# Kernel tuning notes

Measured on AMD Instinct MI355X. Metric: run time of the kernel, lower is better.

Reference implementation:

```python
import jax, jax.numpy as jnp
import numpy as np

IN_FEATURES = 4096
OUT_FEATURES = 4096
BATCH, SEQ = 4, 2048

def setup_inputs() -> dict:
    key = jax.random.key(0)
    k1, k2, k3, k4, k5 = jax.random.split(key, 5)
    x = jax.random.normal(k1, (BATCH, SEQ, IN_FEATURES), dtype=jnp.float32)
    # int8 codes stored as int32 in [0, 255] (asymmetric uint8-style quantization)
    qweight = jax.random.randint(k2, (OUT_FEATURES, IN_FEATURES), 0, 255, dtype=jnp.int32)
    scales = jax.random.uniform(k3, (OUT_FEATURES,), dtype=jnp.float32) * 0.01 + 1e-3
    zero_points = jax.random.uniform(k4, (OUT_FEATURES,), dtype=jnp.float32) * 255.0
    bias = jax.random.normal(k5, (OUT_FEATURES,), dtype=jnp.float32)
    return {"x": x, "qweight": qweight, "scales": scales, "zero_points": zero_points, "bias": bias}

def reference(x, qweight, scales, zero_points, bias):
    # Per-output-channel dequantization: W[o, i] = (q[o, i] - zp[o]) * scale[o]
    w = (qweight.astype(jnp.float32) - zero_points[:, None]) * scales[:, None]  # [O, I]
    # y = x @ W.T + b, fused dequant + GEMM in the original ipex op
    y = jnp.einsum("bsi,oi->bso", x, w) + bias
    return y
```

## Files before the change

### kernel.cpp

```cpp
#include <hip/hip_runtime.h>
#include <hip/hip_bf16.h>

typedef __attribute__((ext_vector_type(4))) int i32x4;
typedef __attribute__((ext_vector_type(16))) int i32x16;

#define M_DIM 8192
#define N_DIM 4096
#define K_DIM 4096
#define BM 256
#define BN 256
#define BK 64
#define NT2 (K_DIM / BK)

static __device__ inline void gload_lds16(const void* g, void* l) {
  __builtin_amdgcn_global_load_lds(
      (const __attribute__((address_space(1))) unsigned int*)g,
      (__attribute__((address_space(3))) unsigned int*)l,
      16, 0, 0);
}

__global__ __launch_bounds__(256) void prep_x_i8(
    const float* __restrict__ x, char* __restrict__ xq,
    float* __restrict__ rx, float* __restrict__ sxf) {
  const int row = blockIdx.x;
  const int tid = threadIdx.x;
  const float4* xr = (const float4*)(x + (long)row * K_DIM);
  float4 v[4];
  float mx = 0.f;
#pragma unroll
  for (int i = 0; i < 4; ++i) {
    v[i] = xr[i * 256 + tid];
    mx = fmaxf(mx, fmaxf(fmaxf(fabsf(v[i].x), fabsf(v[i].y)),
                         fmaxf(fabsf(v[i].z), fabsf(v[i].w))));
  }
#pragma unroll
  for (int off = 32; off > 0; off >>= 1) mx = fmaxf(mx, __shfl_down(mx, off, 64));
  __shared__ float redm[4];
  __shared__ int reds[4];
  const int lane = tid & 63, w = tid >> 6;
  if (lane == 0) redm[w] = mx;
  __syncthreads();
  const float maxv = fmaxf(fmaxf(redm[0], redm[1]), fmaxf(redm[2], redm[3]));
  const float inv = maxv > 0.f ? 127.f / maxv : 0.f;
  int* xo = (int*)(xq + (long)row * K_DIM);
  int ssum = 0;
#pragma unroll
  for (int i = 0; i < 4; ++i) {
    const int q0 = __float2int_rn(v[i].x * inv);
    const int q1 = __float2int_rn(v[i].y * inv);
    const int q2 = __float2int_rn(v[i].z * inv);
    const int q3 = __float2int_rn(v[i].w * inv);
    ssum += q0 + q1 + q2 + q3;
    xo[i * 256 + tid] =
        (q0 & 255) | ((q1 & 255) << 8) | ((q2 & 255) << 16) | ((q3 & 255) << 24);
  }
#pragma unroll
  for (int off = 32; off > 0; off >>= 1) ssum += __shfl_down(ssum, off, 64);
  if (lane == 0) reds[w] = ssum;
  __syncthreads();
  if (tid == 0) {
    rx[row] = maxv * (1.f / 127.f);
    sxf[row] = (float)(reds[0] + reds[1] + reds[2] + reds[3]);
  }
}

__global__ __launch_bounds__(256) void prep_q_i8(
    const int* __restrict__ q, char* __restrict__ qb) {
  const long idx = (long)blockIdx.x * blockDim.x + threadIdx.x;
  const int4 v = ((const int4*)q)[idx];
  const int a = v.x - 128, b = v.y - 128, c = v.z - 128, d = v.w - 128;
  ((int*)qb)[idx] = (a & 255) | ((b & 255) << 8) | ((c & 255) << 16) | ((d & 255) << 24);
}

__global__ __launch_bounds__(512, 2) void wq_gemm_i8(
    const char* __restrict__ A,
    const char* __restrict__ B,
    const float* __restrict__ rx,
    const float* __restrict__ sxf,
    const float* __restrict__ scales,
    const float* __restrict__ zps,
    const float* __restrict__ bias,
    float* __restrict__ C) {
  __shared__ __align__(16) char lds[4 * 32768];

  const int tid = threadIdx.x;
  const int lane = tid & 63;
  const int wv = tid >> 6;
  const int wr = wv >> 2, wc = wv & 3;

  const int wg = blockIdx.x;
  const int lid = (wg & 7) * 64 + (wg >> 3);
  const int bx = lid & 15, by = lid >> 4;
  const int brow = by * BM;
  const int bcol = bx * BN;

  i32x16 acc[4][2] = {};

  const int srow = tid >> 2;
  const int schunk = ((tid & 3) ^ (srow & 3)) * 16;
  const int wub = (tid & ~63) * 16;
  const char* gAs = A + (long)(brow + srow) * K_DIM + schunk;
  const char* gBs = B + (long)(bcol + srow) * K_DIM + schunk;

#define STAGE_A(T)                                                        \
  do {                                                                    \
    char* d = lds + ((T) & 3) * 32768;                                    \
    gload_lds16(gAs + (long)(T) * 64, d + wub);                           \
    gload_lds16(gAs + 524288 + (long)(T) * 64, d + 8192 + wub);           \
  } while (0)
#define STAGE_B(T)                                                        \
  do {                                                                    \
    char* d = lds + ((T) & 3) * 32768 + 16384;                            \
    gload_lds16(gBs + (long)(T) * 64, d + wub);                           \
    gload_lds16(gBs + 524288 + (long)(T) * 64, d + 8192 + wub);           \
  } while (0)

  const int row5 = lane & 31;
  const int kg = lane >> 5;
  int aoff[2], boff[2];
#pragma unroll
  for (int ks = 0; ks < 2; ++ks) {
    const int ch = ((ks * 2 + kg) ^ (row5 & 3)) * 16;
    aoff[ks] = (wr * 128 + row5) * 64 + ch;
    boff[ks] = (wc * 64 + row5) * 64 + ch;
  }

#define RD_A(BB, FM, KS) (*(const i32x4*)(lds + (BB) + aoff[KS] + (FM) * 2048))
#define RD_B(BB, FN, KS) (*(const i32x4*)(lds + (BB) + 16384 + boff[KS] + (FN) * 2048))
#define MMA(FM, FN, AV, BV)                                                   \
  acc[FM][FN] = __builtin_amdgcn_mfma_i32_32x32x32_i8(AV, BV, acc[FM][FN], 0, 0, 0)

#define BAR() __builtin_amdgcn_s_barrier()
#define VMC(N)                                                                \
  do {                                                                        \
    asm volatile("s_waitcnt vmcnt(" #N ")");                                  \
    __builtin_amdgcn_sched_barrier(0);                                        \
  } while (0)

  STAGE_A(0); STAGE_B(0);
  STAGE_A(1); STAGE_B(1);
  VMC(4);
  BAR();

  i32x4 a00, a01, a10, a11, b00, b01, b10, b11;

  for (int t = 0; t < NT2 - 2; ++t) {
    const int bb = (t & 3) * 32768;
    a00 = RD_A(bb, 0, 0); a01 = RD_A(bb, 0, 1);
    a10 = RD_A(bb, 1, 0); a11 = RD_A(bb, 1, 1);
    b00 = RD_B(bb, 0, 0); b01 = RD_B(bb, 0, 1);
    b10 = RD_B(bb, 1, 0); b11 = RD_B(bb, 1, 1);
    STAGE_A(t + 2);
    BAR();
    __builtin_amdgcn_s_setprio(1);
    MMA(0, 0, a00, b00); MMA(0, 1, a00, b10);
    MMA(1, 0, a10, b00); MMA(1, 1, a10, b10);
    MMA(0, 0, a01, b01); MMA(0, 1, a01, b11);
    MMA(1, 0, a11, b01); MMA(1, 1, a11, b11);
    __builtin_amdgcn_s_setprio(0);
    BAR();
    a00 = RD_A(bb, 2, 0); a01 = RD_A(bb, 2, 1);
    a10 = RD_A(bb, 3, 0); a11 = RD_A(bb, 3, 1);
    STAGE_B(t + 2);
    BAR();
    __builtin_amdgcn_s_setprio(1);
    MMA(2, 0, a00, b00); MMA(2, 1, a00, b10);
    MMA(3, 0, a10, b00); MMA(3, 1, a10, b10);
    MMA(2, 0, a01, b01); MMA(2, 1, a01, b11);
    MMA(3, 0, a11, b01); MMA(3, 1, a11, b11);
    __builtin_amdgcn_s_setprio(0);
    VMC(4);
    BAR();
  }

#pragma unroll
  for (int tt = 0; tt < 2; ++tt) {
    const int t = NT2 - 2 + tt;
    const int bb = (t & 3) * 32768;
    a00 = RD_A(bb, 0, 0); a01 = RD_A(bb, 0, 1);
    a10 = RD_A(bb, 1, 0); a11 = RD_A(bb, 1, 1);
    b00 = RD_B(bb, 0, 0); b01 = RD_B(bb, 0, 1);
    b10 = RD_B(bb, 1, 0); b11 = RD_B(bb, 1, 1);
    MMA(0, 0, a00, b00); MMA(0, 1, a00, b10);
    MMA(1, 0, a10, b00); MMA(1, 1, a10, b10);
    MMA(0, 0, a01, b01); MMA(0, 1, a01, b11);
    MMA(1, 0, a11, b01); MMA(1, 1, a11, b11);
    a00 = RD_A(bb, 2, 0); a01 = RD_A(bb, 2, 1);
    a10 = RD_A(bb, 3, 0); a11 = RD_A(bb, 3, 1);
    MMA(2, 0, a00, b00); MMA(2, 1, a00, b10);
    MMA(3, 0, a10, b00); MMA(3, 1, a10, b10);
    MMA(2, 0, a01, b01); MMA(2, 1, a01, b11);
    MMA(3, 0, a11, b01); MMA(3, 1, a11, b11);
    if (tt == 0) { VMC(0); BAR(); }
  }

  float sc[2], zp[2], bs[2];
  int coln[2];
#pragma unroll
  for (int fn = 0; fn < 2; ++fn) {
    coln[fn] = bcol + wc * 64 + fn * 32 + row5;
    sc[fn] = scales[coln[fn]];
    zp[fn] = 128.f - zps[coln[fn]];
    bs[fn] = bias[coln[fn]];
  }
#pragma unroll
  for (int fm = 0; fm < 4; ++fm) {
#pragma unroll
    for (int r = 0; r < 16; ++r) {
      const int grow = brow + wr * 128 + fm * 32 + (r & 3) + 8 * (r >> 2) + 4 * kg;
      const float rxv = rx[grow];
      const float sxv = sxf[grow];
#pragma unroll
      for (int fn = 0; fn < 2; ++fn) {
        C[(long)grow * N_DIM + coln[fn]] =
            sc[fn] * rxv * ((float)acc[fm][fn][r] + zp[fn] * sxv) + bs[fn];
      }
    }
  }
}

extern "C" void kernel_launch(void* const* d_in, const int* in_sizes, int n_in,
                              void* d_out, int out_size, void* d_ws, size_t ws_size,
                              hipStream_t stream) {
  const float* x = (const float*)d_in[0];
  const int* qw = (const int*)d_in[1];
  const float* scales = (const float*)d_in[2];
  const float* zps = (const float*)d_in[3];
  const float* bias = (const float*)d_in[4];
  float* out = (float*)d_out;

  char* ws = (char*)d_ws;
  char* xq = ws;
  char* qb = ws + (size_t)32 * 1024 * 1024;
  float* rx = (float*)(ws + (size_t)48 * 1024 * 1024);
  float* sxf = (float*)(ws + (size_t)48 * 1024 * 1024 + 65536);

  hipLaunchKernelGGL(prep_x_i8, dim3(M_DIM), dim3(256), 0, stream, x, xq, rx, sxf);
  hipLaunchKernelGGL(prep_q_i8, dim3((N_DIM * K_DIM / 4) / 256), dim3(256), 0, stream,
                     qw, qb);
  hipLaunchKernelGGL(wq_gemm_i8, dim3((M_DIM / BM) * (N_DIM / BN)), dim3(512), 0,
                     stream, xq, qb, rx, sxf, scales, zps, bias, out);
}
```

Measured before the change: 215.6 us.

## Double K tile to 128 with two-stage LDS ring and finer-grained staging

Raises the GEMM K-tile from 64 to 128 and switches the LDS ring from four 32KB stages to two 64KB stages, with an 8-way XOR swizzle to match the wider rows. Each iteration now runs four MMA phases, and the global-to-LDS loads for the next tile are split into four quarter-stages placed between them. The aim is to halve the number of loop iterations and barriers per K element and to spread memory traffic more evenly across the compute. The cost is a shallower prefetch distance (one tile ahead instead of two), more live B registers, and subtler vmcnt and barrier ordering that could stall or race.

```diff
diff --git a/kernel.cpp b/kernel.cpp
--- a/kernel.cpp
+++ b/kernel.cpp
@@ -9,7 +9,7 @@
 #define K_DIM 4096
 #define BM 256
 #define BN 256
-#define BK 64
+#define BK 128
 #define NT2 (K_DIM / BK)
 
 static __device__ inline void gload_lds16(const void* g, void* l) {
@@ -81,7 +81,7 @@
     const float* __restrict__ zps,
     const float* __restrict__ bias,
     float* __restrict__ C) {
-  __shared__ __align__(16) char lds[4 * 32768];
+  __shared__ __align__(16) char lds[2 * 65536];
 
   const int tid = threadIdx.x;
   const int lane = tid & 63;
@@ -96,37 +96,41 @@
 
   i32x16 acc[4][2] = {};
 
-  const int srow = tid >> 2;
-  const int schunk = ((tid & 3) ^ (srow & 3)) * 16;
+  const int srow = tid >> 3;
+  const int schunk = ((tid & 7) ^ (srow & 7)) * 16;
   const int wub = (tid & ~63) * 16;
   const char* gAs = A + (long)(brow + srow) * K_DIM + schunk;
   const char* gBs = B + (long)(bcol + srow) * K_DIM + schunk;
 
-#define STAGE_A(T)                                                        \
-  do {                                                                    \
-    char* d = lds + ((T) & 3) * 32768;                                    \
-    gload_lds16(gAs + (long)(T) * 64, d + wub);                           \
-    gload_lds16(gAs + 524288 + (long)(T) * 64, d + 8192 + wub);           \
+#define STAGE_A2(T, J0, J1)                                                   \
+  do {                                                                        \
+    char* d = lds + ((T) & 1) * 65536;                                        \
+    gload_lds16(gAs + (long)(J0) * 262144 + (long)(T) * 128,                  \
+                d + (J0) * 8192 + wub);                                       \
+    gload_lds16(gAs + (long)(J1) * 262144 + (long)(T) * 128,                  \
+                d + (J1) * 8192 + wub);                                       \
   } while (0)
-#define STAGE_B(T)                                                        \
-  do {                                                                    \
-    char* d = lds + ((T) & 3) * 32768 + 16384;                            \
-    gload_lds16(gBs + (long)(T) * 64, d + wub);                           \
-    gload_lds16(gBs + 524288 + (long)(T) * 64, d + 8192 + wub);           \
+#define STAGE_B2(T, J0, J1)                                                   \
+  do {                                                                        \
+    char* d = lds + ((T) & 1) * 65536 + 32768;                                \
+    gload_lds16(gBs + (long)(J0) * 262144 + (long)(T) * 128,                  \
+                d + (J0) * 8192 + wub);                                       \
+    gload_lds16(gBs + (long)(J1) * 262144 + (long)(T) * 128,                  \
+                d + (J1) * 8192 + wub);                                       \
   } while (0)
 
   const int row5 = lane & 31;
   const int kg = lane >> 5;
-  int aoff[2], boff[2];
-#pragma unroll
-  for (int ks = 0; ks < 2; ++ks) {
-    const int ch = ((ks * 2 + kg) ^ (row5 & 3)) * 16;
-    aoff[ks] = (wr * 128 + row5) * 64 + ch;
-    boff[ks] = (wc * 64 + row5) * 64 + ch;
-  }
-
-#define RD_A(BB, FM, KS) (*(const i32x4*)(lds + (BB) + aoff[KS] + (FM) * 2048))
-#define RD_B(BB, FN, KS) (*(const i32x4*)(lds + (BB) + 16384 + boff[KS] + (FN) * 2048))
+  int aoff[4], boff[4];
+#pragma unroll
+  for (int ks = 0; ks < 4; ++ks) {
+    const int ch = ((ks * 2 + kg) ^ (row5 & 7)) * 16;
+    aoff[ks] = (wr * 128 + row5) * 128 + ch;
+    boff[ks] = (wc * 64 + row5) * 128 + ch;
+  }
+
+#define RD_A(BB, FM, KS) (*(const i32x4*)(lds + (BB) + aoff[KS] + (FM) * 4096))
+#define RD_B(BB, FN, KS) (*(const i32x4*)(lds + (BB) + 32768 + boff[KS] + (FN) * 4096))
 #define MMA(FM, FN, AV, BV)                                                   \
   acc[FM][FN] = __builtin_amdgcn_mfma_i32_32x32x32_i8(AV, BV, acc[FM][FN], 0, 0, 0)
 
@@ -137,20 +141,23 @@
     __builtin_amdgcn_sched_barrier(0);                                        \
   } while (0)
 
-  STAGE_A(0); STAGE_B(0);
-  STAGE_A(1); STAGE_B(1);
-  VMC(4);
+  STAGE_A2(0, 0, 2);
+  STAGE_B2(0, 0, 2);
+  STAGE_B2(0, 1, 3);
+  STAGE_A2(0, 1, 3);
+  VMC(2);
   BAR();
 
-  i32x4 a00, a01, a10, a11, b00, b01, b10, b11;
-
-  for (int t = 0; t < NT2 - 2; ++t) {
-    const int bb = (t & 3) * 32768;
-    a00 = RD_A(bb, 0, 0); a01 = RD_A(bb, 0, 1);
-    a10 = RD_A(bb, 1, 0); a11 = RD_A(bb, 1, 1);
-    b00 = RD_B(bb, 0, 0); b01 = RD_B(bb, 0, 1);
-    b10 = RD_B(bb, 1, 0); b11 = RD_B(bb, 1, 1);
-    STAGE_A(t + 2);
+  i32x4 a00, a01, a10, a11, b00, b10, b01, b11, b02, b12, b03, b13;
+
+  for (int t = 0; t < NT2 - 1; ++t) {
+    const int bb = (t & 1) * 65536;
+    const int t1 = t + 1;
+    a00 = RD_A(bb, 0, 0); a10 = RD_A(bb, 1, 0);
+    a01 = RD_A(bb, 0, 1); a11 = RD_A(bb, 1, 1);
+    b00 = RD_B(bb, 0, 0); b10 = RD_B(bb, 1, 0);
+    b01 = RD_B(bb, 0, 1); b11 = RD_B(bb, 1, 1);
+    STAGE_A2(t1, 0, 2);
     BAR();
     __builtin_amdgcn_s_setprio(1);
     MMA(0, 0, a00, b00); MMA(0, 1, a00, b10);
@@ -159,9 +166,23 @@
     MMA(1, 0, a11, b01); MMA(1, 1, a11, b11);
     __builtin_amdgcn_s_setprio(0);
     BAR();
-    a00 = RD_A(bb, 2, 0); a01 = RD_A(bb, 2, 1);
-    a10 = RD_A(bb, 3, 0); a11 = RD_A(bb, 3, 1);
-    STAGE_B(t + 2);
+    a00 = RD_A(bb, 0, 2); a10 = RD_A(bb, 1, 2);
+    a01 = RD_A(bb, 0, 3); a11 = RD_A(bb, 1, 3);
+    b02 = RD_B(bb, 0, 2); b12 = RD_B(bb, 1, 2);
+    b03 = RD_B(bb, 0, 3); b13 = RD_B(bb, 1, 3);
+    STAGE_B2(t1, 0, 2);
+    BAR();
+    __builtin_amdgcn_s_setprio(1);
+    MMA(0, 0, a00, b02); MMA(0, 1, a00, b12);
+    MMA(1, 0, a10, b02); MMA(1, 1, a10, b12);
+    MMA(0, 0, a01, b03); MMA(0, 1, a01, b13);
+    MMA(1, 0, a11, b03); MMA(1, 1, a11, b13);
+    __builtin_amdgcn_s_setprio(0);
+    VMC(4);
+    BAR();
+    a00 = RD_A(bb, 2, 0); a10 = RD_A(bb, 3, 0);
+    a01 = RD_A(bb, 2, 1); a11 = RD_A(bb, 3, 1);
+    STAGE_B2(t1, 1, 3);
     BAR();
     __builtin_amdgcn_s_setprio(1);
     MMA(2, 0, a00, b00); MMA(2, 1, a00, b10);
@@ -169,29 +190,53 @@
     MMA(2, 0, a01, b01); MMA(2, 1, a01, b11);
     MMA(3, 0, a11, b01); MMA(3, 1, a11, b11);
     __builtin_amdgcn_s_setprio(0);
-    VMC(4);
-    BAR();
-  }
-
-#pragma unroll
-  for (int tt = 0; tt < 2; ++tt) {
-    const int t = NT2 - 2 + tt;
-    const int bb = (t & 3) * 32768;
-    a00 = RD_A(bb, 0, 0); a01 = RD_A(bb, 0, 1);
-    a10 = RD_A(bb, 1, 0); a11 = RD_A(bb, 1, 1);
-    b00 = RD_B(bb, 0, 0); b01 = RD_B(bb, 0, 1);
-    b10 = RD_B(bb, 1, 0); b11 = RD_B(bb, 1, 1);
+    BAR();
+    a00 = RD_A(bb, 2, 2); a10 = RD_A(bb, 3, 2);
+    a01 = RD_A(bb, 2, 3); a11 = RD_A(bb, 3, 3);
+    STAGE_A2(t1, 1, 3);
+    BAR();
+    __builtin_amdgcn_s_setprio(1);
+    MMA(2, 0, a00, b02); MMA(2, 1, a00, b12);
+    MMA(3, 0, a10, b02); MMA(3, 1, a10, b12);
+    MMA(2, 0, a01, b03); MMA(2, 1, a01, b13);
+    MMA(3, 0, a11, b03); MMA(3, 1, a11, b13);
+    __builtin_amdgcn_s_setprio(0);
+    VMC(2);
+    BAR();
+  }
+
+  {
+    const int bb = 65536;
+    a00 = RD_A(bb, 0, 0); a10 = RD_A(bb, 1, 0);
+    a01 = RD_A(bb, 0, 1); a11 = RD_A(bb, 1, 1);
+    b00 = RD_B(bb, 0, 0); b10 = RD_B(bb, 1, 0);
+    b01 = RD_B(bb, 0, 1); b11 = RD_B(bb, 1, 1);
     MMA(0, 0, a00, b00); MMA(0, 1, a00, b10);
     MMA(1, 0, a10, b00); MMA(1, 1, a10, b10);
     MMA(0, 0, a01, b01); MMA(0, 1, a01, b11);
     MMA(1, 0, a11, b01); MMA(1, 1, a11, b11);
-    a00 = RD_A(bb, 2, 0); a01 = RD_A(bb, 2, 1);
-    a10 = RD_A(bb, 3, 0); a11 = RD_A(bb, 3, 1);
+    a00 = RD_A(bb, 0, 2); a10 = RD_A(bb, 1, 2);
+    a01 = RD_A(bb, 0, 3); a11 = RD_A(bb, 1, 3);
+    b02 = RD_B(bb, 0, 2); b12 = RD_B(bb, 1, 2);
+    b03 = RD_B(bb, 0, 3); b13 = RD_B(bb, 1, 3);
+    MMA(0, 0, a00, b02); MMA(0, 1, a00, b12);
+    MMA(1, 0, a10, b02); MMA(1, 1, a10, b12);
+    MMA(0, 0, a01, b03); MMA(0, 1, a01, b13);
+    MMA(1, 0, a11, b03); MMA(1, 1, a11, b13);
+    VMC(0);
+    BAR();
+    a00 = RD_A(bb, 2, 0); a10 = RD_A(bb, 3, 0);
+    a01 = RD_A(bb, 2, 1); a11 = RD_A(bb, 3, 1);
     MMA(2, 0, a00, b00); MMA(2, 1, a00, b10);
     MMA(3, 0, a10, b00); MMA(3, 1, a10, b10);
     MMA(2, 0, a01, b01); MMA(2, 1, a01, b11);
     MMA(3, 0, a11, b01); MMA(3, 1, a11, b11);
-    if (tt == 0) { VMC(0); BAR(); }
+    a00 = RD_A(bb, 2, 2); a10 = RD_A(bb, 3, 2);
+    a01 = RD_A(bb, 2, 3); a11 = RD_A(bb, 3, 3);
+    MMA(2, 0, a00, b02); MMA(2, 1, a00, b12);
+    MMA(3, 0, a10, b02); MMA(3, 1, a10, b12);
+    MMA(2, 0, a01, b03); MMA(2, 1, a01, b13);
+    MMA(3, 0, a11, b03); MMA(3, 1, a11, b13);
   }
 
   float sc[2], zp[2], bs[2];
```

Measured after the change: 195.5 us. -9.4%, faster.
